# Kernel optimization log

Measured on AMD Instinct MI355X. Metric: run time of the kernel, lower is better.

## Reference

```python
import jax, jax.numpy as jnp
import numpy as np

EPS = 1e-5  # torch InstanceNorm1d default eps

def _inst_norm(x, gamma, beta):
    # x: [B,S,D]; torch InstanceNorm1d normalizes over seq axis per channel (biased var)
    mu = x.mean(axis=1, keepdims=True)
    var = x.var(axis=1, keepdims=True)
    return (x - mu) / jnp.sqrt(var + EPS) * gamma + beta

def _encoder_layer(x, neg_dist, log_scale, Wq, Wk, Wv, alpha, g1, b1, W1, bW1, W2, bW2, g2, b2):
    q = x @ Wq.T
    k = x @ Wk.T
    v = x @ Wv.T
    s = log_scale * alpha * neg_dist            # [B,S,S]
    es = jnp.exp(s)
    ek = jnp.exp(k)                             # [B,S,D]
    num = es @ (ek * v)                         # [B,S,D]
    den = es @ ek                               # [B,S,D]
    weighted = jnp.nan_to_num(num) / jnp.nan_to_num(den)
    aft = jax.nn.sigmoid(q) * weighted
    h = _inst_norm(x + aft, g1, b1)
    ff = jax.nn.relu(h @ W1.T + bW1) @ W2.T + bW2
    return _inst_norm(h + ff, g2, b2)

def setup_inputs() -> dict:
    key = jax.random.key(0)
    B, N, D, F, L = 32, 999, 128, 512, 6
    ks = jax.random.split(key, 32)
    n = lambda i, shape, s: (jax.random.normal(ks[i], shape, dtype=jnp.float32) * s)
    inp = {
        "depot_xy": jax.random.uniform(ks[0], (B, 1, 2), dtype=jnp.float32),
        "node_xy_demand": jax.random.uniform(ks[1], (B, N, 3), dtype=jnp.float32),
        "dist": jax.random.uniform(ks[2], (B, N + 1, N + 1), dtype=jnp.float32),
        "log_scale": jnp.ones((1,), dtype=jnp.float32),
        "flag": jax.random.randint(ks[3], (B,), 0, 2, dtype=jnp.int32),
        # embedding params
        "Wd": n(4, (D, 2), 0.1), "bd": jnp.zeros((D,), jnp.float32),
        "Wn": n(5, (D, 3), 0.1), "bn": jnp.zeros((D,), jnp.float32),
        "Win": n(6, (D, D), 0.05), "bin_": jnp.zeros((D,), jnp.float32),
        "Wout": n(7, (D, D), 0.05), "bout": jnp.zeros((D,), jnp.float32),
        # stacked per-layer params
        "Wq": n(8, (L, D, D), 0.05), "Wk": n(9, (L, D, D), 0.05), "Wv": n(10, (L, D, D), 0.05),
        "alpha": jnp.ones((L,), jnp.float32),
        "g1": jnp.ones((L, D), jnp.float32), "b1": jnp.zeros((L, D), jnp.float32),
        "W1": n(11, (L, F, D), 0.05), "bW1": jnp.zeros((L, F), jnp.float32),
        "W2": n(12, (L, D, F), 0.05), "bW2": jnp.zeros((L, D), jnp.float32),
        "g2": jnp.ones((L, D), jnp.float32), "b2": jnp.zeros((L, D), jnp.float32),
    }
    return inp

def reference(depot_xy, node_xy_demand, dist, log_scale, flag,
              Wd, bd, Wn, bn, Win, bin_, Wout, bout,
              Wq, Wk, Wv, alpha, g1, b1, W1, bW1, W2, bW2, g2, b2):
    B, N, _ = node_xy_demand.shape
    ed = depot_xy @ Wd.T + bd                    # [B,1,D]
    en = node_xy_demand @ Wn.T + bn              # [B,N,D]
    en = en.at[:, 0, :].set(en[:, 0, :] @ Win.T + bin_)
    out = jnp.concatenate([ed, en], axis=1)      # [B,N+1,D]
    idx = ((1 - flag) * N).astype(jnp.int32)     # index 0 or N per batch
    rows = jnp.arange(B)
    last = out[rows, idx] @ Wout.T + bout        # [B,D]
    out = out.at[rows, idx].set(last)
    neg_dist = -dist
    for i in range(Wq.shape[0]):
        out = _encoder_layer(out, neg_dist, log_scale,
                             Wq[i], Wk[i], Wv[i], alpha[i],
                             g1[i], b1[i], W1[i], bW1[i], W2[i], bW2[i], g2[i], b2[i])
    return out
```

## Files before the change

### kernel.cpp

```cpp
#include <hip/hip_runtime.h>
#include <hip/hip_bf16.h>
#include <float.h>
#include <math.h>

#define B 32
#define NN 999
#define S 1000
#define D 128
#define F 512
#define L 6
#define EPSN 1e-5f
#define WSTR 180224

typedef __attribute__((ext_vector_type(4))) float f32x4;
typedef __attribute__((ext_vector_type(4))) short s16x4;
typedef __attribute__((ext_vector_type(8))) short s16x8;

#if defined(__has_builtin)
#if __has_builtin(__builtin_amdgcn_mfma_f32_16x16x16bf16_1k)
#define HAVE_MFMA16 1
#endif
#if __has_builtin(__builtin_amdgcn_mfma_f32_16x16x32_bf16)
#define HAVE_MFMA32 1
#endif
#endif

#ifdef HAVE_MFMA16
#define MFMA16(a, b, c) __builtin_amdgcn_mfma_f32_16x16x16bf16_1k((a), (b), (c), 0, 0, 0)
#else
static __device__ __forceinline__ f32x4 mfma16_asm(s16x4 a, s16x4 b, f32x4 c) {
    asm volatile("v_mfma_f32_16x16x16_bf16 %0, %1, %2, %0\n\ts_nop 7\n\ts_nop 7"
                 : "+v"(c) : "v"(a), "v"(b));
    return c;
}
#define MFMA16(a, b, c) mfma16_asm((a), (b), (c))
#endif

#ifdef HAVE_MFMA32
#define MFMA32(a, b, c) __builtin_amdgcn_mfma_f32_16x16x32_bf16((a), (b), (c), 0, 0, 0)
#else
static __device__ __forceinline__ f32x4 mfma32_asm(s16x8 a, s16x8 b, f32x4 c) {
    asm volatile("v_mfma_f32_16x16x32_bf16 %0, %1, %2, %0\n\ts_nop 7\n\ts_nop 7"
                 : "+v"(c) : "v"(a), "v"(b));
    return c;
}
#define MFMA32(a, b, c) mfma32_asm((a), (b), (c))
#endif

__device__ __forceinline__ float n2n(float v) {
    if (v != v) return 0.f;
    if (isinf(v)) return v > 0.f ? FLT_MAX : -FLT_MAX;
    return v;
}

__device__ __forceinline__ unsigned short f2bf(float x) {
    unsigned u = __float_as_uint(x);
    return (unsigned short)((u + 0x7fffu + ((u >> 16) & 1u)) >> 16);
}

__device__ __forceinline__ float bf2f(unsigned short v) {
    return __uint_as_float(((unsigned)v) << 16);
}

__global__ __launch_bounds__(256) void k_wprep(
        const float* __restrict__ Wq, const float* __restrict__ Wk,
        const float* __restrict__ Wv, const float* __restrict__ W1,
        const float* __restrict__ W2, unsigned short* __restrict__ wbf) {
    int bx = blockIdx.x, l = blockIdx.y;
    const float* src; int doff, off;
    if (bx < 8)       { src = Wq + (size_t)l * 16384; doff = 0;      off = bx * 2048; }
    else if (bx < 16) { src = Wk + (size_t)l * 16384; doff = 16384;  off = (bx - 8) * 2048; }
    else if (bx < 24) { src = Wv + (size_t)l * 16384; doff = 32768;  off = (bx - 16) * 2048; }
    else if (bx < 56) { src = W1 + (size_t)l * 65536; doff = 49152;  off = (bx - 24) * 2048; }
    else              { src = W2 + (size_t)l * 65536; doff = 114688; off = (bx - 56) * 2048; }
    int i = off + threadIdx.x * 8;
    float4 a4 = *(const float4*)(src + i);
    float4 b4 = *(const float4*)(src + i + 4);
    s16x8 p = {(short)f2bf(a4.x), (short)f2bf(a4.y), (short)f2bf(a4.z), (short)f2bf(a4.w),
               (short)f2bf(b4.x), (short)f2bf(b4.y), (short)f2bf(b4.z), (short)f2bf(b4.w)};
    *(s16x8*)(wbf + (size_t)l * WSTR + doff + i) = p;
}

__global__ __launch_bounds__(256) void k_prep(
        const float* __restrict__ dist, unsigned short* __restrict__ nd) {
    int row = blockIdx.x;
    int col = threadIdx.x * 4;
    unsigned short* op = nd + (size_t)row * 1024 + col;
    if (col < 1000) {
        float4 v = *(const float4*)(dist + (size_t)row * 1000 + col);
        s16x4 p = {(short)f2bf(v.x), (short)f2bf(v.y), (short)f2bf(v.z), (short)f2bf(v.w)};
        *(s16x4*)op = p;
    } else {
        s16x4 z = {0, 0, 0, 0};
        *(s16x4*)op = z;
    }
}

__global__ __launch_bounds__(128) void k_embed(
        const float* __restrict__ depot, const float* __restrict__ node,
        const float* __restrict__ Wd, const float* __restrict__ bd,
        const float* __restrict__ Wn, const float* __restrict__ bn,
        float* __restrict__ x) {
    int row = blockIdx.x;
    int b = row / S, s = row % S;
    int d = threadIdx.x;
    float o;
    if (s == 0) {
        float x0 = depot[b * 2 + 0], x1 = depot[b * 2 + 1];
        o = Wd[d * 2 + 0] * x0 + Wd[d * 2 + 1] * x1 + bd[d];
    } else {
        const float* p = node + ((size_t)b * NN + (s - 1)) * 3;
        o = Wn[d * 3 + 0] * p[0] + Wn[d * 3 + 1] * p[1] + Wn[d * 3 + 2] * p[2] + bn[d];
    }
    x[(size_t)row * D + d] = o;
}

__global__ __launch_bounds__(128) void k_rowxform(
        float* __restrict__ x, const float* __restrict__ W,
        const float* __restrict__ bias, const int* __restrict__ flag, int mode) {
    int b = blockIdx.x;
    int d = threadIdx.x;
    __shared__ float row[D];
    int r = (mode == 0) ? 1 : (1 - flag[b]) * NN;
    float* xr = x + ((size_t)b * S + r) * D;
    row[d] = xr[d];
    __syncthreads();
    float acc = bias[d];
    for (int e = 0; e < D; e += 4) {
        const float4 w = *(const float4*)(W + (size_t)d * D + e);
        acc += w.x * row[e] + w.y * row[e + 1] + w.z * row[e + 2] + w.w * row[e + 3];
    }
    xr[d] = acc;
}

__global__ __launch_bounds__(256) void k_qkv(
        const float* __restrict__ yprev, const float* __restrict__ part2, int hasnorm,
        const float* __restrict__ gp, const float* __restrict__ bp,
        const unsigned short* __restrict__ wl,
        unsigned short* __restrict__ sqb, unsigned short* __restrict__ mT) {
    int blk = blockIdx.x;
    int b = blk >> 4, rb = blk & 15;
    int s0 = rb * 64;
    int tid = threadIdx.x, lane = tid & 63, wid = tid >> 6;
    __shared__ __align__(16) unsigned short lds[18432];
    __shared__ float nsc[128], nsh[128];
    __shared__ float accv[256];
    unsigned short* xs = lds;
    unsigned short* wt0 = lds + 2560;

    if (hasnorm) {
        int st = tid >> 7, d = tid & 127;
        float s = 0.f;
#pragma unroll
        for (int c = 0; c < 16; c++) s += part2[(size_t)(b * 32 + c * 2 + st) * 128 + d];
        accv[tid] = s;
    }
    __syncthreads();
    if (tid < 128) {
        float scv = 1.f, shv = 0.f;
        if (hasnorm) {
            float mu = accv[tid] * (1.f / S);
            float var = accv[128 + tid] * (1.f / S) - mu * mu;
            float rs = rsqrtf(var + EPSN);
            scv = rs * gp[tid];
            shv = bp[tid] - mu * scv;
        }
        nsc[tid] = scv; nsh[tid] = shv;
    }
    __syncthreads();

    f32x4 acc[3][8];
#pragma unroll
    for (int mm = 0; mm < 3; mm++)
#pragma unroll
        for (int cf = 0; cf < 8; cf++) acc[mm][cf] = {0.f, 0.f, 0.f, 0.f};

    for (int k0 = 0; k0 < D; k0 += 32) {
        {
            int i = tid >> 2, kq = (tid & 3) * 8;
            int s = s0 + i;
            int gs = s < S ? s : S - 1;
            const float* gpx = yprev + ((size_t)b * S + gs) * D + k0 + kq;
            float4 a4 = *(const float4*)gpx;
            float4 b4 = *(const float4*)(gpx + 4);
            const float* scp = &nsc[k0 + kq];
            const float* shp = &nsh[k0 + kq];
            s16x4 p0 = {(short)f2bf(a4.x * scp[0] + shp[0]), (short)f2bf(a4.y * scp[1] + shp[1]),
                        (short)f2bf(a4.z * scp[2] + shp[2]), (short)f2bf(a4.w * scp[3] + shp[3])};
            s16x4 p1 = {(short)f2bf(b4.x * scp[4] + shp[4]), (short)f2bf(b4.y * scp[5] + shp[5]),
                        (short)f2bf(b4.z * scp[6] + shp[6]), (short)f2bf(b4.w * scp[7] + shp[7])};
            *(s16x4*)&xs[i * 40 + kq] = p0;
            *(s16x4*)&xs[i * 40 + kq + 4] = p1;
        }
#pragma unroll
        for (int u0 = 0; u0 < 6; u0++) {
            int u = tid + u0 * 256;
            int mm = u >> 9;
            int v = u & 511;
            int c = v >> 2, kq = (v & 3) * 8;
            s16x8 w = *(const s16x8*)(wl + (size_t)mm * 16384 + (size_t)c * D + k0 + kq);
            *(s16x8*)&wt0[mm * 5120 + c * 40 + kq] = w;
        }
        __syncthreads();
#pragma unroll
        for (int ks = 0; ks < 2; ks++) {
            int ko = ks * 16 + (lane >> 4) * 4;
            s16x4 a = *(const s16x4*)&xs[(wid * 16 + (lane & 15)) * 40 + ko];
#pragma unroll
            for (int mm = 0; mm < 3; mm++)
#pragma unroll
                for (int cf = 0; cf < 8; cf++) {
                    s16x4 bf = *(const s16x4*)&wt0[mm * 5120 + (cf * 16 + (lane & 15)) * 40 + ko];
                    acc[mm][cf] = MFMA16(a, bf, acc[mm][cf]);
                }
        }
        __syncthreads();
    }

    unsigned short* tile = lds;
    int sl0 = wid * 16 + (lane >> 4) * 4;
#pragma unroll
    for (int cf = 0; cf < 8; cf++) {
        int d = cf * 16 + (lane & 15);
        s16x4 p0, p1;
#pragma unroll
        for (int r = 0; r < 4; r++) {
            int s = s0 + sl0 + r;
            if (s < S) {
                float qv = acc[0][cf][r], kv = acc[1][cf][r], vv = acc[2][cf][r];
                float ek = __expf(kv);
                sqb[((size_t)b * S + s) * D + d] = f2bf(1.f / (1.f + __expf(-qv)));
                p0[r] = (short)f2bf(ek * vv);
                p1[r] = (short)f2bf(ek);
            } else { p0[r] = 0; p1[r] = 0; }
        }
        *(s16x4*)&tile[d * 72 + sl0] = p0;
        *(s16x4*)&tile[(d + 128) * 72 + sl0] = p1;
    }
    __syncthreads();
    {
        unsigned short* base = mT + (((size_t)b * 16 + rb) * 256) * 64;
#pragma unroll
        for (int j = 0; j < 8; j++) {
            int u = j * 256 + tid;
            int d = u >> 3, sp = u & 7;
            int o = sp ^ (d & 7);
            s16x8 v = *(const s16x8*)&tile[d * 72 + o * 8];
            *(s16x8*)(base + (size_t)u * 8) = v;
        }
    }
}

__global__ __launch_bounds__(256) void k_attn(
        const float* __restrict__ yprev, const float* __restrict__ part2, int hasnorm,
        const float* __restrict__ gp, const float* __restrict__ bp,
        const unsigned short* __restrict__ sqb,
        const unsigned short* __restrict__ mT, const unsigned short* __restrict__ nd,
        const float* __restrict__ log_scale, const float* __restrict__ alpha, int l,
        float* __restrict__ y, float* __restrict__ part) {
    int blk0 = blockIdx.x;
    int blk = (blk0 & 7) * 64 + (blk0 >> 3);
    int b = blk >> 4, ib = blk & 15;
    int i0 = ib * 64;
    int tid = threadIdx.x, lane = tid & 63, wid = tid >> 6;
    __shared__ __align__(16) unsigned short esL[64 * 64];
    __shared__ __align__(16) unsigned short mtL[256 * 64];
    __shared__ float accvA[256];
    float sc = log_scale[0] * alpha[l];

    if (hasnorm) {
        int st = tid >> 7, d = tid & 127;
        float s = 0.f;
#pragma unroll
        for (int c = 0; c < 16; c++) s += part2[(size_t)(b * 32 + c * 2 + st) * 128 + d];
        accvA[tid] = s;
    }
    __syncthreads();

    float rsc[8], rsh[8];
#pragma unroll
    for (int cf = 0; cf < 8; cf++) {
        int d = cf * 16 + (lane & 15);
        float scv = 1.f, shv = 0.f;
        if (hasnorm) {
            float mu = accvA[d] * (1.f / S);
            float var = accvA[128 + d] * (1.f / S) - mu * mu;
            float rs = rsqrtf(var + EPSN);
            scv = rs * gp[d];
            shv = bp[d] - mu * scv;
        }
        rsc[cf] = scv; rsh[cf] = shv;
    }

    f32x4 acc[16];
#pragma unroll
    for (int cf = 0; cf < 16; cf++) acc[cf] = {0.f, 0.f, 0.f, 0.f};

    int erow = tid >> 2;
    int gi = i0 + erow; if (gi > 999) gi = 999;
    const unsigned short* ndr = nd + (size_t)b * 1000 * 1024 + (size_t)gi * 1024 + (tid & 3) * 16;
    const unsigned short* mtb = mT + (size_t)b * 16 * 16384;
    int eg = (tid & 3) * 2;
    unsigned short* esw0 = &esL[erow * 64 + ((eg) ^ (erow & 7)) * 8];
    unsigned short* esw1 = &esL[erow * 64 + ((eg + 1) ^ (erow & 7)) * 8];

    s16x8 cnA = *(const s16x8*)(ndr);
    s16x8 cnB = *(const s16x8*)(ndr + 8);
    s16x8 cm[8];
#pragma unroll
    for (int i2 = 0; i2 < 8; i2++)
        cm[i2] = *(const s16x8*)(mtb + (size_t)(i2 * 256 + tid) * 8);

    for (int kc = 0; kc < 16; kc++) {
        s16x8 o0, o1;
#pragma unroll
        for (int j = 0; j < 8; j++) {
            o0[j] = (short)f2bf(__expf(-sc * bf2f((unsigned short)cnA[j])));
            o1[j] = (short)f2bf(__expf(-sc * bf2f((unsigned short)cnB[j])));
        }
        int kn = kc < 15 ? kc + 1 : 15;
        cnA = *(const s16x8*)(ndr + kn * 64);
        cnB = *(const s16x8*)(ndr + kn * 64 + 8);
        __syncthreads();
        *(s16x8*)esw0 = o0;
        *(s16x8*)esw1 = o1;
#pragma unroll
        for (int i2 = 0; i2 < 8; i2++)
            *(s16x8*)&mtL[(i2 * 256 + tid) * 8] = cm[i2];
#pragma unroll
        for (int i2 = 0; i2 < 8; i2++)
            cm[i2] = *(const s16x8*)(mtb + (size_t)kn * 16384 + (size_t)(i2 * 256 + tid) * 8);
        __syncthreads();
#pragma unroll
        for (int ks = 0; ks < 2; ks++) {
            int arow = wid * 16 + (lane & 15);
            int ag = ks * 4 + (lane >> 4);
            s16x8 a = *(const s16x8*)&esL[arow * 64 + ((ag ^ (arow & 7)) * 8)];
            __builtin_amdgcn_s_setprio(1);
#pragma unroll
            for (int cf = 0; cf < 16; cf++) {
                int c = (cf & 7) * 16 + (cf >> 3) * 128 + (lane & 15);
                s16x8 bf = *(const s16x8*)&mtL[c * 64 + ((ag ^ (c & 7)) * 8)];
                acc[cf] = MFMA32(a, bf, acc[cf]);
            }
            __builtin_amdgcn_s_setprio(0);
        }
    }

    __syncthreads();
    float* pw = (float*)mtL;
#pragma unroll
    for (int cf = 0; cf < 8; cf++) {
        int d = cf * 16 + (lane & 15);
        float s = 0.f, s2 = 0.f;
#pragma unroll
        for (int r = 0; r < 4; r++) {
            int i = i0 + wid * 16 + (lane >> 4) * 4 + r;
            if (i < S) {
                size_t off = ((size_t)b * S + i) * D + d;
                float w = n2n(acc[cf][r]) / n2n(acc[cf + 8][r]);
                float xv = yprev[off] * rsc[cf] + rsh[cf];
                float yv = xv + bf2f(sqb[off]) * w;
                y[off] = yv;
                s += yv;
                s2 = fmaf(yv, yv, s2);
            }
        }
        s += __shfl_xor(s, 16); s += __shfl_xor(s, 32);
        s2 += __shfl_xor(s2, 16); s2 += __shfl_xor(s2, 32);
        if (lane < 16) {
            pw[(wid * 2 + 0) * 128 + d] = s;
            pw[(wid * 2 + 1) * 128 + d] = s2;
        }
    }
    __syncthreads();
    {
        int st = tid >> 7, d = tid & 127;
        float v = pw[(0 * 2 + st) * 128 + d] + pw[(1 * 2 + st) * 128 + d] +
                  pw[(2 * 2 + st) * 128 + d] + pw[(3 * 2 + st) * 128 + d];
        part[((size_t)(b * 16 + ib) * 2 + st) * 128 + d] = v;
    }
}

__global__ __launch_bounds__(256) void k_ffn(
        const float* __restrict__ ya, const float* __restrict__ part1,
        const float* __restrict__ gp, const float* __restrict__ bp,
        const unsigned short* __restrict__ w1b, const unsigned short* __restrict__ w2b,
        const float* __restrict__ bW1, const float* __restrict__ bW2,
        float* __restrict__ yb, float* __restrict__ part) {
    int blk = blockIdx.x;
    int b = blk >> 4, rb = blk & 15;
    int r0 = rb * 64;
    int tid = threadIdx.x, lane = tid & 63, wid = tid >> 6;
    __shared__ __align__(16) unsigned short hs[64 * 128];
    __shared__ __align__(16) unsigned short w1c[64 * 128];
    __shared__ __align__(16) unsigned short tc[64 * 72];
    __shared__ __align__(16) unsigned short w2c[128 * 64];
    __shared__ float nsc[128], nsh[128];
    __shared__ float accv[256];

    {
        int st = tid >> 7, d = tid & 127;
        float s = 0.f;
#pragma unroll
        for (int c = 0; c < 16; c++) s += part1[(size_t)(b * 32 + c * 2 + st) * 128 + d];
        accv[tid] = s;
    }
    __syncthreads();
    if (tid < 128) {
        float mu = accv[tid] * (1.f / S);
        float var = accv[128 + tid] * (1.f / S) - mu * mu;
        float rs = rsqrtf(var + EPSN);
        float scv = rs * gp[tid];
        nsc[tid] = scv;
        nsh[tid] = bp[tid] - mu * scv;
    }
    __syncthreads();

    {
        int i = tid >> 2;
        int gs = r0 + i; if (gs >= S) gs = S - 1;
        const float* gpx = ya + ((size_t)b * S + gs) * D;
#pragma unroll
        for (int q = 0; q < 4; q++) {
            int col = (tid & 3) * 32 + q * 8;
            int g = col >> 3;
            float4 a4 = *(const float4*)(gpx + col);
            float4 b4 = *(const float4*)(gpx + col + 4);
            const float* scp = &nsc[col];
            const float* shp = &nsh[col];
            s16x4 p0 = {(short)f2bf(a4.x * scp[0] + shp[0]), (short)f2bf(a4.y * scp[1] + shp[1]),
                        (short)f2bf(a4.z * scp[2] + shp[2]), (short)f2bf(a4.w * scp[3] + shp[3])};
            s16x4 p1 = {(short)f2bf(b4.x * scp[4] + shp[4]), (short)f2bf(b4.y * scp[5] + shp[5]),
                        (short)f2bf(b4.z * scp[6] + shp[6]), (short)f2bf(b4.w * scp[7] + shp[7])};
            int base = i * 128 + ((g ^ (i & 7)) * 8);
            *(s16x4*)&hs[base] = p0;
            *(s16x4*)&hs[base + 4] = p1;
        }
    }

    f32x4 yacc[8];
#pragma unroll
    for (int cf = 0; cf < 8; cf++) yacc[cf] = {0.f, 0.f, 0.f, 0.f};

    for (int fc = 0; fc < 8; fc++) {
        int c0 = fc * 64;
        {
            int f = tid >> 2;
#pragma unroll
            for (int q = 0; q < 4; q++) {
                int col = (tid & 3) * 32 + q * 8;
                int g = col >> 3;
                s16x8 w = *(const s16x8*)(w1b + (size_t)(c0 + f) * D + col);
                *(s16x8*)&w1c[f * 128 + ((g ^ (f & 7)) * 8)] = w;
            }
        }
        {
            int d2 = tid >> 1;
#pragma unroll
            for (int q = 0; q < 4; q++) {
                int g = (tid & 1) * 4 + q;
                s16x8 w = *(const s16x8*)(w2b + (size_t)d2 * F + c0 + g * 8);
                *(s16x8*)&w2c[d2 * 64 + ((g ^ (d2 & 7)) * 8)] = w;
            }
        }
        __syncthreads();
        f32x4 tacc[4];
#pragma unroll
        for (int c4 = 0; c4 < 4; c4++) tacc[c4] = {0.f, 0.f, 0.f, 0.f};
#pragma unroll
        for (int ks = 0; ks < 4; ks++) {
            int g = ks * 4 + (lane >> 4);
            int arow = wid * 16 + (lane & 15);
            s16x8 a = *(const s16x8*)&hs[arow * 128 + ((g ^ (arow & 7)) * 8)];
#pragma unroll
            for (int c4 = 0; c4 < 4; c4++) {
                int brow = c4 * 16 + (lane & 15);
                s16x8 bf = *(const s16x8*)&w1c[brow * 128 + ((g ^ (brow & 7)) * 8)];
                tacc[c4] = MFMA32(a, bf, tacc[c4]);
            }
        }
#pragma unroll
        for (int c4 = 0; c4 < 4; c4++) {
            int col = c4 * 16 + (lane & 15);
            float bias = bW1[c0 + col];
#pragma unroll
            for (int r = 0; r < 4; r++) {
                int rl = wid * 16 + (lane >> 4) * 4 + r;
                tc[rl * 72 + col] = f2bf(fmaxf(tacc[c4][r] + bias, 0.f));
            }
        }
        __syncthreads();
#pragma unroll
        for (int ks = 0; ks < 2; ks++) {
            int ko = ks * 32 + (lane >> 4) * 8;
            int g = ks * 4 + (lane >> 4);
            s16x8 a = *(const s16x8*)&tc[(wid * 16 + (lane & 15)) * 72 + ko];
#pragma unroll
            for (int cf = 0; cf < 8; cf++) {
                int brow = cf * 16 + (lane & 15);
                s16x8 bf = *(const s16x8*)&w2c[brow * 64 + ((g ^ (brow & 7)) * 8)];
                yacc[cf] = MFMA32(a, bf, yacc[cf]);
            }
        }
        __syncthreads();
    }

    float* pw = (float*)w1c;
#pragma unroll
    for (int cf = 0; cf < 8; cf++) {
        int d = cf * 16 + (lane & 15);
        float bias = bW2[d];
        float s = 0.f, s2 = 0.f;
#pragma unroll
        for (int r = 0; r < 4; r++) {
            int rl = wid * 16 + (lane >> 4) * 4 + r;
            int row = r0 + rl;
            if (row < S) {
                float hval = bf2f(hs[rl * 128 + (((d >> 3) ^ (rl & 7)) * 8) + (d & 7)]);
                float yv = hval + yacc[cf][r] + bias;
                yb[((size_t)b * S + row) * D + d] = yv;
                s += yv;
                s2 = fmaf(yv, yv, s2);
            }
        }
        s += __shfl_xor(s, 16); s += __shfl_xor(s, 32);
        s2 += __shfl_xor(s2, 16); s2 += __shfl_xor(s2, 32);
        if (lane < 16) {
            pw[(wid * 2 + 0) * 128 + d] = s;
            pw[(wid * 2 + 1) * 128 + d] = s2;
        }
    }
    __syncthreads();
    {
        int st = tid >> 7, d = tid & 127;
        float v = pw[(0 * 2 + st) * 128 + d] + pw[(1 * 2 + st) * 128 + d] +
                  pw[(2 * 2 + st) * 128 + d] + pw[(3 * 2 + st) * 128 + d];
        part[((size_t)(b * 16 + rb) * 2 + st) * 128 + d] = v;
    }
}

__global__ __launch_bounds__(256) void k_finalize(
        const float* __restrict__ part, float* __restrict__ acc) {
    int i = blockIdx.x * 256 + threadIdx.x;
    int b = i >> 8, k = i & 255;
    float s = 0.f;
#pragma unroll
    for (int c = 0; c < 16; c++) s += part[(size_t)(b * 16 + c) * 256 + k];
    acc[i] = s;
}

__global__ __launch_bounds__(256) void k_norm(
        const float* __restrict__ y, const float* __restrict__ acc,
        const float* __restrict__ g, const float* __restrict__ bb,
        float* __restrict__ out) {
    size_t i = (size_t)blockIdx.x * 256 + threadIdx.x;
    int d = (int)(i % D);
    int b = (int)(i / ((size_t)S * D));
    float mu = acc[b * 256 + d] * (1.f / S);
    float var = acc[b * 256 + 128 + d] * (1.f / S) - mu * mu;
    float v = (y[i] - mu) * rsqrtf(var + EPSN);
    out[i] = v * g[d] + bb[d];
}

extern "C" void kernel_launch(void* const* d_in, const int* in_sizes, int n_in,
                              void* d_out, int out_size, void* d_ws, size_t ws_size,
                              hipStream_t stream) {
    const float* depot = (const float*)d_in[0];
    const float* node  = (const float*)d_in[1];
    const float* dist  = (const float*)d_in[2];
    const float* log_scale = (const float*)d_in[3];
    const int*   flag  = (const int*)d_in[4];
    const float* Wd   = (const float*)d_in[5];
    const float* bd   = (const float*)d_in[6];
    const float* Wn   = (const float*)d_in[7];
    const float* bn   = (const float*)d_in[8];
    const float* Win  = (const float*)d_in[9];
    const float* bin_ = (const float*)d_in[10];
    const float* Wout = (const float*)d_in[11];
    const float* bout = (const float*)d_in[12];
    const float* Wq   = (const float*)d_in[13];
    const float* Wk   = (const float*)d_in[14];
    const float* Wv   = (const float*)d_in[15];
    const float* alpha= (const float*)d_in[16];
    const float* g1   = (const float*)d_in[17];
    const float* b1   = (const float*)d_in[18];
    const float* W1   = (const float*)d_in[19];
    const float* bW1  = (const float*)d_in[20];
    const float* W2   = (const float*)d_in[21];
    const float* bW2  = (const float*)d_in[22];
    const float* g2   = (const float*)d_in[23];
    const float* b2   = (const float*)d_in[24];

    float* ws = (float*)d_ws;
    size_t nxd = (size_t)B * S * D;
    float* ya    = ws;
    float* yb    = ws + nxd;
    float* part1 = ws + 2 * nxd;
    float* part2 = part1 + 131072;
    float* accb2 = part2 + 131072;
    unsigned short* sqb = (unsigned short*)(accb2 + 8192);
    unsigned short* mT  = sqb + nxd;
    unsigned short* wbf = mT + (size_t)B * 16 * 256 * 64;
    unsigned short* nd  = wbf + (size_t)L * WSTR;

    k_wprep<<<dim3(88, 6), 256, 0, stream>>>(Wq, Wk, Wv, W1, W2, wbf);
    k_prep<<<B * S, 256, 0, stream>>>(dist, nd);
    k_embed<<<B * S, 128, 0, stream>>>(depot, node, Wd, bd, Wn, bn, yb);
    k_rowxform<<<B, 128, 0, stream>>>(yb, Win, bin_, flag, 0);
    k_rowxform<<<B, 128, 0, stream>>>(yb, Wout, bout, flag, 1);

    for (int l = 0; l < L; l++) {
        int hasnorm = (l > 0) ? 1 : 0;
        const float* gpn = g2 + (l > 0 ? (l - 1) : 0) * D;
        const float* bpn = b2 + (l > 0 ? (l - 1) : 0) * D;
        const unsigned short* wl = wbf + (size_t)l * WSTR;
        k_qkv<<<B * 16, 256, 0, stream>>>(yb, part2, hasnorm, gpn, bpn, wl, sqb, mT);
        k_attn<<<B * 16, 256, 0, stream>>>(yb, part2, hasnorm, gpn, bpn,
                                           sqb, mT, nd, log_scale, alpha, l, ya, part1);
        k_ffn<<<B * 16, 256, 0, stream>>>(ya, part1, g1 + l * D, b1 + l * D,
                                          wl + 49152, wl + 114688,
                                          bW1 + (size_t)l * F, bW2 + (size_t)l * D, yb, part2);
    }
    k_finalize<<<32, 256, 0, stream>>>(part2, accb2);
    k_norm<<<B * S * D / 256, 256, 0, stream>>>(yb, accb2, g2 + 5 * D, b2 + 5 * D, (float*)d_out);
}
```

Measured before the change: 665.3 us.

## Split attention kernel across 8 waves, one half per numerator/denominator

The attention kernel now runs 512 threads per block. Waves 0-3 compute the numerator columns and waves 4-7 the denominator columns, so each wave keeps 8 accumulator fragments instead of 16. Staging loads are spread over twice as many threads, and the denominator half hands its results to the numerator half through shared memory before the epilogue. This aims to lower register pressure and raise MFMA-issuing waves per CU, at the cost of an extra shared-memory round trip and barrier and an epilogue handled by only half the waves.

```diff
diff --git a/kernel.cpp b/kernel.cpp
--- a/kernel.cpp
+++ b/kernel.cpp
@@ -251,7 +251,7 @@
     }
 }
 
-__global__ __launch_bounds__(256) void k_attn(
+__global__ __launch_bounds__(512, 2) void k_attn(
         const float* __restrict__ yprev, const float* __restrict__ part2, int hasnorm,
         const float* __restrict__ gp, const float* __restrict__ bp,
         const unsigned short* __restrict__ sqb,
@@ -263,12 +263,13 @@
     int b = blk >> 4, ib = blk & 15;
     int i0 = ib * 64;
     int tid = threadIdx.x, lane = tid & 63, wid = tid >> 6;
+    int wr = wid & 3, wh = wid >> 2;
     __shared__ __align__(16) unsigned short esL[64 * 64];
     __shared__ __align__(16) unsigned short mtL[256 * 64];
     __shared__ float accvA[256];
     float sc = log_scale[0] * alpha[l];
 
-    if (hasnorm) {
+    if (hasnorm && tid < 256) {
         int st = tid >> 7, d = tid & 127;
         float s = 0.f;
 #pragma unroll
@@ -292,54 +293,47 @@
         rsc[cf] = scv; rsh[cf] = shv;
     }
 
-    f32x4 acc[16];
-#pragma unroll
-    for (int cf = 0; cf < 16; cf++) acc[cf] = {0.f, 0.f, 0.f, 0.f};
-
-    int erow = tid >> 2;
+    f32x4 acc[8];
+#pragma unroll
+    for (int cf = 0; cf < 8; cf++) acc[cf] = {0.f, 0.f, 0.f, 0.f};
+
+    int erow = tid >> 3, og = tid & 7;
     int gi = i0 + erow; if (gi > 999) gi = 999;
-    const unsigned short* ndr = nd + (size_t)b * 1000 * 1024 + (size_t)gi * 1024 + (tid & 3) * 16;
+    const unsigned short* ndr = nd + (size_t)b * 1000 * 1024 + (size_t)gi * 1024 + og * 8;
     const unsigned short* mtb = mT + (size_t)b * 16 * 16384;
-    int eg = (tid & 3) * 2;
-    unsigned short* esw0 = &esL[erow * 64 + ((eg) ^ (erow & 7)) * 8];
-    unsigned short* esw1 = &esL[erow * 64 + ((eg + 1) ^ (erow & 7)) * 8];
-
-    s16x8 cnA = *(const s16x8*)(ndr);
-    s16x8 cnB = *(const s16x8*)(ndr + 8);
-    s16x8 cm[8];
-#pragma unroll
-    for (int i2 = 0; i2 < 8; i2++)
-        cm[i2] = *(const s16x8*)(mtb + (size_t)(i2 * 256 + tid) * 8);
+    unsigned short* esw = &esL[erow * 64 + ((og ^ (erow & 7)) * 8)];
+
+    s16x8 cn = *(const s16x8*)(ndr);
+    s16x8 cm[4];
+#pragma unroll
+    for (int j = 0; j < 4; j++)
+        cm[j] = *(const s16x8*)(mtb + (size_t)(j * 512 + tid) * 8);
 
     for (int kc = 0; kc < 16; kc++) {
-        s16x8 o0, o1;
-#pragma unroll
-        for (int j = 0; j < 8; j++) {
-            o0[j] = (short)f2bf(__expf(-sc * bf2f((unsigned short)cnA[j])));
-            o1[j] = (short)f2bf(__expf(-sc * bf2f((unsigned short)cnB[j])));
-        }
+        s16x8 o0;
+#pragma unroll
+        for (int j = 0; j < 8; j++)
+            o0[j] = (short)f2bf(__expf(-sc * bf2f((unsigned short)cn[j])));
         int kn = kc < 15 ? kc + 1 : 15;
-        cnA = *(const s16x8*)(ndr + kn * 64);
-        cnB = *(const s16x8*)(ndr + kn * 64 + 8);
+        cn = *(const s16x8*)(ndr + kn * 64);
         __syncthreads();
-        *(s16x8*)esw0 = o0;
-        *(s16x8*)esw1 = o1;
-#pragma unroll
-        for (int i2 = 0; i2 < 8; i2++)
-            *(s16x8*)&mtL[(i2 * 256 + tid) * 8] = cm[i2];
-#pragma unroll
-        for (int i2 = 0; i2 < 8; i2++)
-            cm[i2] = *(const s16x8*)(mtb + (size_t)kn * 16384 + (size_t)(i2 * 256 + tid) * 8);
+        *(s16x8*)esw = o0;
+#pragma unroll
+        for (int j = 0; j < 4; j++)
+            *(s16x8*)&mtL[(j * 512 + tid) * 8] = cm[j];
+#pragma unroll
+        for (int j = 0; j < 4; j++)
+            cm[j] = *(const s16x8*)(mtb + (size_t)kn * 16384 + (size_t)(j * 512 + tid) * 8);
         __syncthreads();
 #pragma unroll
         for (int ks = 0; ks < 2; ks++) {
-            int arow = wid * 16 + (lane & 15);
+            int arow = wr * 16 + (lane & 15);
             int ag = ks * 4 + (lane >> 4);
             s16x8 a = *(const s16x8*)&esL[arow * 64 + ((ag ^ (arow & 7)) * 8)];
             __builtin_amdgcn_s_setprio(1);
 #pragma unroll
-            for (int cf = 0; cf < 16; cf++) {
-                int c = (cf & 7) * 16 + (cf >> 3) * 128 + (lane & 15);
+            for (int cf = 0; cf < 8; cf++) {
+                int c = cf * 16 + wh * 128 + (lane & 15);
                 s16x8 bf = *(const s16x8*)&mtL[c * 64 + ((ag ^ (c & 7)) * 8)];
                 acc[cf] = MFMA32(a, bf, acc[cf]);
             }
@@ -349,35 +343,51 @@
 
     __syncthreads();
     float* pw = (float*)mtL;
-#pragma unroll
-    for (int cf = 0; cf < 8; cf++) {
-        int d = cf * 16 + (lane & 15);
-        float s = 0.f, s2 = 0.f;
-#pragma unroll
-        for (int r = 0; r < 4; r++) {
-            int i = i0 + wid * 16 + (lane >> 4) * 4 + r;
-            if (i < S) {
-                size_t off = ((size_t)b * S + i) * D + d;
-                float w = n2n(acc[cf][r]) / n2n(acc[cf + 8][r]);
-                float xv = yprev[off] * rsc[cf] + rsh[cf];
-                float yv = xv + bf2f(sqb[off]) * w;
-                y[off] = yv;
-                s += yv;
-                s2 = fmaf(yv, yv, s2);
-            }
-        }
-        s += __shfl_xor(s, 16); s += __shfl_xor(s, 32);
-        s2 += __shfl_xor(s2, 16); s2 += __shfl_xor(s2, 32);
-        if (lane < 16) {
-            pw[(wid * 2 + 0) * 128 + d] = s;
-            pw[(wid * 2 + 1) * 128 + d] = s2;
-        }
-    }
-    __syncthreads();
-    {
+    if (wh == 1) {
+#pragma unroll
+        for (int cf = 0; cf < 8; cf++) {
+            int c = cf * 16 + (lane & 15);
+#pragma unroll
+            for (int r = 0; r < 4; r++) {
+                int rl = wr * 16 + (lane >> 4) * 4 + r;
+                pw[rl * 128 + c] = acc[cf][r];
+            }
+        }
+    }
+    __syncthreads();
+    float* sw = (float*)esL;
+    if (wh == 0) {
+#pragma unroll
+        for (int cf = 0; cf < 8; cf++) {
+            int d = cf * 16 + (lane & 15);
+            float s = 0.f, s2 = 0.f;
+#pragma unroll
+            for (int r = 0; r < 4; r++) {
+                int rl = wr * 16 + (lane >> 4) * 4 + r;
+                int i = i0 + rl;
+                if (i < S) {
+                    size_t off = ((size_t)b * S + i) * D + d;
+                    float w = n2n(acc[cf][r]) / n2n(pw[rl * 128 + d]);
+                    float xv = yprev[off] * rsc[cf] + rsh[cf];
+                    float yv = xv + bf2f(sqb[off]) * w;
+                    y[off] = yv;
+                    s += yv;
+                    s2 = fmaf(yv, yv, s2);
+                }
+            }
+            s += __shfl_xor(s, 16); s += __shfl_xor(s, 32);
+            s2 += __shfl_xor(s2, 16); s2 += __shfl_xor(s2, 32);
+            if (lane < 16) {
+                sw[(wr * 2 + 0) * 128 + d] = s;
+                sw[(wr * 2 + 1) * 128 + d] = s2;
+            }
+        }
+    }
+    __syncthreads();
+    if (tid < 256) {
         int st = tid >> 7, d = tid & 127;
-        float v = pw[(0 * 2 + st) * 128 + d] + pw[(1 * 2 + st) * 128 + d] +
-                  pw[(2 * 2 + st) * 128 + d] + pw[(3 * 2 + st) * 128 + d];
+        float v = sw[(0 * 2 + st) * 128 + d] + sw[(1 * 2 + st) * 128 + d] +
+                  sw[(2 * 2 + st) * 128 + d] + sw[(3 * 2 + st) * 128 + d];
         part[((size_t)(b * 16 + ib) * 2 + st) * 128 + d] = v;
     }
 }
@@ -616,7 +626,7 @@
         const float* bpn = b2 + (l > 0 ? (l - 1) : 0) * D;
         const unsigned short* wl = wbf + (size_t)l * WSTR;
         k_qkv<<<B * 16, 256, 0, stream>>>(yb, part2, hasnorm, gpn, bpn, wl, sqb, mT);
-        k_attn<<<B * 16, 256, 0, stream>>>(yb, part2, hasnorm, gpn, bpn,
+        k_attn<<<B * 16, 512, 0, stream>>>(yb, part2, hasnorm, gpn, bpn,
                                            sqb, mT, nd, log_scale, alpha, l, ya, part1);
         k_ffn<<<B * 16, 256, 0, stream>>>(ya, part1, g1 + l * D, b1 + l * D,
                                           wl + 49152, wl + 114688,
```

After: 643.0 us. 3.4% less time.
